# Kernel tuning notes

Hardware: AMD Instinct MI355X
Metric: run time of the kernel (lower is better)

## Reference

```python
import jax, jax.numpy as jnp
import numpy as np

VOCAB, EMBED, HID = 10, 256, 512
B, S, T = 8, 1024, 256  # Senc = S // 4 = 256


def _conv1d(x, w, b):
    # x: (B, Cin, L), w: (Cout, Cin, 3), padding=1 -> same length
    y = jax.lax.conv_general_dilated(x, w, window_strides=(1,), padding=[(1, 1)],
                                     dimension_numbers=('NCH', 'OIH', 'NCH'))
    return y + b[None, :, None]


def _maxpool2(x):
    # MaxPool1d(kernel=2, stride=2) on (B, C, L)
    b, c, l = x.shape
    return x.reshape(b, c, l // 2, 2).max(axis=-1)


def _lstm_layer(x, wih, whh, bih, bhh):
    # x: (B, T, Din); PyTorch gate order i, f, g, o; zero initial state
    b, t, _ = x.shape
    h_dim = whh.shape[1]
    xg = x @ wih.T + (bih + bhh)  # (B, T, 4H) - input projection hoisted out of scan

    def step(carry, xt):
        h, c = carry
        gates = xt + h @ whh.T
        i, f, g, o = jnp.split(gates, 4, axis=-1)
        c = jax.nn.sigmoid(f) * c + jax.nn.sigmoid(i) * jnp.tanh(g)
        h = jax.nn.sigmoid(o) * jnp.tanh(c)
        return (h, c), h

    init = (jnp.zeros((b, h_dim), x.dtype), jnp.zeros((b, h_dim), x.dtype))
    _, hs = jax.lax.scan(step, init, jnp.swapaxes(xg, 0, 1))
    return jnp.swapaxes(hs, 0, 1)  # (B, T, H)


def setup_inputs() -> dict:
    key = jax.random.key(0)
    ks = jax.random.split(key, 24)

    def unif(k, shape, fan_in):
        bound = 1.0 / np.sqrt(fan_in)
        return jax.random.uniform(k, shape, jnp.float32, -bound, bound)

    inp = {
        'src': jax.random.randint(ks[0], (B, S), 0, VOCAB),
        'tgt': jax.random.randint(ks[1], (B, T), 0, VOCAB),
        'embedding': jax.random.normal(ks[2], (VOCAB, EMBED), jnp.float32),
        'conv1_w': unif(ks[3], (256, EMBED, 3), EMBED * 3),
        'conv1_b': unif(ks[4], (256,), EMBED * 3),
        'conv2_w': unif(ks[5], (512, 256, 3), 256 * 3),
        'conv2_b': unif(ks[6], (512,), 256 * 3),
        'conv3_w': unif(ks[7], (512, 512, 3), 512 * 3),
        'conv3_b': unif(ks[8], (512,), 512 * 3),
        'lstm0_wih': unif(ks[9], (4 * HID, EMBED), HID),
        'lstm0_whh': unif(ks[10], (4 * HID, HID), HID),
        'lstm0_bih': unif(ks[11], (4 * HID,), HID),
        'lstm0_bhh': unif(ks[12], (4 * HID,), HID),
        'lstm1_wih': unif(ks[13], (4 * HID, HID), HID),
        'lstm1_whh': unif(ks[14], (4 * HID, HID), HID),
        'lstm1_bih': unif(ks[15], (4 * HID,), HID),
        'lstm1_bhh': unif(ks[16], (4 * HID,), HID),
        'attn_w': unif(ks[17], (1, 2 * HID), 2 * HID),
        'attn_b': unif(ks[18], (1,), 2 * HID),
        'out_w': unif(ks[19], (VOCAB, HID), HID),
        'out_b': unif(ks[20], (VOCAB,), HID),
    }
    return inp


def reference(src, tgt, embedding, conv1_w, conv1_b, conv2_w, conv2_b, conv3_w, conv3_b,
              lstm0_wih, lstm0_whh, lstm0_bih, lstm0_bhh,
              lstm1_wih, lstm1_whh, lstm1_bih, lstm1_bhh,
              attn_w, attn_b, out_w, out_b):
    # --- CNN encoder ---
    x = jnp.swapaxes(embedding[src], 1, 2)          # (B, E, S)
    x = _maxpool2(jax.nn.relu(_conv1d(x, conv1_w, conv1_b)))
    x = _maxpool2(jax.nn.relu(_conv1d(x, conv2_w, conv2_b)))
    x = jax.nn.relu(_conv1d(x, conv3_w, conv3_b))
    enc = jnp.swapaxes(x, 1, 2)                     # (B, Senc, 512)

    # --- LSTM decoder (2 layers) ---
    h = _lstm_layer(embedding[tgt], lstm0_wih, lstm0_whh, lstm0_bih, lstm0_bhh)
    dec = _lstm_layer(h, lstm1_wih, lstm1_whh, lstm1_bih, lstm1_bhh)  # (B, T, 512)

    # --- Bahdanau-style attention ---
    # Linear(cat([dec, enc])) == dec @ W[:, :H].T + enc @ W[:, H:].T + b,
    # so broadcast the two rank-1 projections instead of materializing (B,T,Senc,1024).
    dec_p = jnp.einsum('bth,h->bt', dec, attn_w[0, :HID])   # (B, T)
    enc_p = jnp.einsum('bsh,h->bs', enc, attn_w[0, HID:])   # (B, Senc)
    scores = dec_p[:, :, None] + enc_p[:, None, :] + attn_b[0]  # (B, T, Senc)
    attn = jax.nn.softmax(scores, axis=2)
    context = jnp.einsum('bts,bsd->btd', attn, enc)         # (B, T, 512)

    output = dec @ out_w.T + out_b                          # (B, T, VOCAB)
    # Original module computes context then discards it; we return it too so the
    # attention workload is not dead-code-eliminated under jit.
    return output, context
```

## Files before the change

### kernel.cpp

```cpp
#include <hip/hip_runtime.h>
#include <cstddef>

constexpr int OXB0 = 0;
constexpr int OXB1 = OXB0 + 8 * 1026 * 256;
constexpr int OXB2 = OXB1 + 8 * 514 * 256;
constexpr int OENC = OXB2 + 8 * 258 * 512;
constexpr int OWR1 = OENC + 8 * 256 * 512;
constexpr int OWR2 = OWR1 + 768 * 256;
constexpr int OWR3 = OWR2 + 768 * 512;
constexpr int OWR0 = OWR3 + 1536 * 512;
constexpr int OTGT = OWR0 + 256 * 2048;
constexpr int OXG0 = OTGT + 2048 * 256;
constexpr int OH0S = OXG0 + 2048 * 2048;
constexpr int OH1S = OH0S + 257 * 4096;
constexpr int OCTX = OH1S + 257 * 4096;
constexpr int OFLG = OCTX + 8 * 512;

constexpr int FSTR = 16;
constexpr unsigned SENT = 0x7FC0DEADu;

__device__ __forceinline__ float hsum4(const float4& a) { return a.x + a.y + a.z + a.w; }
__device__ __forceinline__ float4 relu4(float4 v, const float4& bv) {
    v.x = fmaxf(v.x + bv.x, 0.f); v.y = fmaxf(v.y + bv.y, 0.f);
    v.z = fmaxf(v.z + bv.z, 0.f); v.w = fmaxf(v.w + bv.w, 0.f); return v;
}
__device__ __forceinline__ float4 max4(const float4& a, const float4& b) {
    float4 r; r.x = fmaxf(a.x, b.x); r.y = fmaxf(a.y, b.y);
    r.z = fmaxf(a.z, b.z); r.w = fmaxf(a.w, b.w); return r;
}
__device__ __forceinline__ float sigmf(float x) { return 1.f / (1.f + expf(-x)); }
__device__ __forceinline__ void fma4(float4& acc, const float4& a, const float4& b) {
    acc.x = fmaf(a.x, b.x, acc.x); acc.y = fmaf(a.y, b.y, acc.y);
    acc.z = fmaf(a.z, b.z, acc.z); acc.w = fmaf(a.w, b.w, acc.w);
}

__device__ __forceinline__ unsigned long long aload64(const float* p) {
    return __hip_atomic_load((const unsigned long long*)p, __ATOMIC_RELAXED,
                             __HIP_MEMORY_SCOPE_AGENT);
}
__device__ __forceinline__ void astore32(float* p, float v) {
    __hip_atomic_store((unsigned int*)p, __float_as_uint(v), __ATOMIC_RELAXED,
                       __HIP_MEMORY_SCOPE_AGENT);
}
__device__ __forceinline__ int aloadi(const int* p) {
    return __hip_atomic_load(p, __ATOMIC_RELAXED, __HIP_MEMORY_SCOPE_AGENT);
}
__device__ __forceinline__ void astorei(int* p, int v) {
    __hip_atomic_store(p, v, __ATOMIC_RELAXED, __HIP_MEMORY_SCOPE_AGENT);
}
__device__ __forceinline__ float2 unpack64(unsigned long long v) {
    float2 f;
    f.x = __uint_as_float((unsigned)v);
    f.y = __uint_as_float((unsigned)(v >> 32));
    return f;
}
__device__ __forceinline__ unsigned sent_in(unsigned long long v) {
    return ((unsigned)v == SENT) | ((unsigned)(v >> 32) == SENT);
}

__global__ void init_kernel(float* __restrict__ ws, int* __restrict__ flags) {
    int idx = blockIdx.x * 256 + threadIdx.x;
    int stride = gridDim.x * 256;
    float sentf = __uint_as_float(SENT);
    for (int i = idx; i < 257 * 4096; i += stride) {
        float v = (i < 4096) ? 0.f : sentf;
        ws[OH0S + i] = v;
        ws[OH1S + i] = v;
    }
    for (int i = idx; i < 192 * FSTR; i += stride) flags[i] = 0;
    for (int i = idx; i < 8 * 2 * 256; i += stride) {
        int b = i >> 9, rr = (i >> 8) & 1, c = i & 255;
        ws[OXB1 + b * 131584 + (rr ? 513 : 0) * 256 + c] = 0.f;
    }
    for (int i = idx; i < 8 * 2 * 512; i += stride) {
        int b = i >> 10, rr = (i >> 9) & 1, c = i & 511;
        ws[OXB2 + b * 132096 + (rr ? 257 : 0) * 512 + c] = 0.f;
    }
}

__global__ void embed_src_kernel(const int* __restrict__ src, const float* __restrict__ emb,
                                 float* __restrict__ xb0) {
    int fi = blockIdx.x * 256 + threadIdx.x;
    int e4 = fi & 63;
    int r = fi >> 6;
    int b = r / 1026;
    int p = r - b * 1026;
    float4 v = make_float4(0.f, 0.f, 0.f, 0.f);
    if (p > 0 && p < 1025) {
        int row = src[b * 1024 + (p - 1)];
        v = *(const float4*)(emb + row * 256 + e4 * 4);
    }
    *(float4*)(xb0 + (size_t)fi * 4) = v;
}

__global__ void gather_tgt_kernel(const int* __restrict__ tgt, const float* __restrict__ emb,
                                  float* __restrict__ et) {
    int fi = blockIdx.x * 256 + threadIdx.x;
    int e4 = fi & 63;
    int r = fi >> 6;
    int t = r >> 3, b = r & 7;
    int row = tgt[b * 256 + t];
    *(float4*)(et + (size_t)fi * 4) = *(const float4*)(emb + row * 256 + e4 * 4);
}

__global__ void tr_conv_kernel(const float* __restrict__ w, float* __restrict__ wr,
                               int Cout, int Cin) {
    int idx = blockIdx.x * 256 + threadIdx.x;
    int co = idx / (Cin * 3);
    int rem = idx - co * Cin * 3;
    int ci = rem / 3;
    int dk = rem - ci * 3;
    wr[(dk * Cin + ci) * Cout + co] = w[idx];
}
__global__ void tr_mat_kernel(const float* __restrict__ w, float* __restrict__ wr,
                              int N, int K) {
    int idx = blockIdx.x * 256 + threadIdx.x;
    int n = idx / K;
    int k = idx - n * K;
    wr[k * N + n] = w[idx];
}

__launch_bounds__(256)
__global__ void gemm_kernel(const float* __restrict__ A, int aBS, int RS, int K,
                            const float* __restrict__ Bw, int N,
                            const float* __restrict__ bias, const float* __restrict__ bias2,
                            float* __restrict__ out, int oBS, int mode) {
    __shared__ float As[32 * 68];
    __shared__ float Bs[32 * 64];
    const int tid = threadIdx.x;
    const int tl = tid & 15, tco = tid >> 4;
    const int m0 = blockIdx.x * 64, n0 = blockIdx.y * 64;
    const int b = blockIdx.z;
    const float* Ab = A + (size_t)b * aBS;
    float4 acc0 = make_float4(0, 0, 0, 0), acc1 = acc0, acc2 = acc0, acc3 = acc0;

    for (int k0 = 0; k0 < K; k0 += 32) {
#pragma unroll
        for (int p = 0; p < 2; ++p) {
            int f = p * 256 + tid;
            int row = f >> 3, j4 = f & 7;
            float4 av = *(const float4*)(Ab + (size_t)(m0 + row) * RS + k0 + j4 * 4);
            int kb = j4 * 4;
            As[(kb + 0) * 68 + row] = av.x;
            As[(kb + 1) * 68 + row] = av.y;
            As[(kb + 2) * 68 + row] = av.z;
            As[(kb + 3) * 68 + row] = av.w;
        }
#pragma unroll
        for (int p = 0; p < 2; ++p) {
            int f = p * 256 + tid;
            int kk = f >> 4, j4 = f & 15;
            *(float4*)(&Bs[kk * 64 + j4 * 4]) =
                *(const float4*)(Bw + (size_t)(k0 + kk) * N + n0 + j4 * 4);
        }
        __syncthreads();
#pragma unroll
        for (int kk = 0; kk < 32; ++kk) {
            float4 a4 = *(const float4*)(&As[kk * 68 + tl * 4]);
            float4 b4 = *(const float4*)(&Bs[kk * 64 + tco * 4]);
            acc0.x = fmaf(a4.x, b4.x, acc0.x); acc0.y = fmaf(a4.x, b4.y, acc0.y);
            acc0.z = fmaf(a4.x, b4.z, acc0.z); acc0.w = fmaf(a4.x, b4.w, acc0.w);
            acc1.x = fmaf(a4.y, b4.x, acc1.x); acc1.y = fmaf(a4.y, b4.y, acc1.y);
            acc1.z = fmaf(a4.y, b4.z, acc1.z); acc1.w = fmaf(a4.y, b4.w, acc1.w);
            acc2.x = fmaf(a4.z, b4.x, acc2.x); acc2.y = fmaf(a4.z, b4.y, acc2.y);
            acc2.z = fmaf(a4.z, b4.z, acc2.z); acc2.w = fmaf(a4.z, b4.w, acc2.w);
            acc3.x = fmaf(a4.w, b4.x, acc3.x); acc3.y = fmaf(a4.w, b4.y, acc3.y);
            acc3.z = fmaf(a4.w, b4.z, acc3.z); acc3.w = fmaf(a4.w, b4.w, acc3.w);
        }
        __syncthreads();
    }

    int nb = n0 + tco * 4;
    float4 bv;
    bv.x = bias[nb + 0]; bv.y = bias[nb + 1]; bv.z = bias[nb + 2]; bv.w = bias[nb + 3];
    if (bias2) { bv.x += bias2[nb + 0]; bv.y += bias2[nb + 1]; bv.z += bias2[nb + 2]; bv.w += bias2[nb + 3]; }

    if (mode == 0) {
        float4 v0 = acc0, v1 = acc1, v2 = acc2, v3 = acc3;
        v0.x += bv.x; v0.y += bv.y; v0.z += bv.z; v0.w += bv.w;
        v1.x += bv.x; v1.y += bv.y; v1.z += bv.z; v1.w += bv.w;
        v2.x += bv.x; v2.y += bv.y; v2.z += bv.z; v2.w += bv.w;
        v3.x += bv.x; v3.y += bv.y; v3.z += bv.z; v3.w += bv.w;
        int mr = m0 + tl * 4;
        *(float4*)(out + (size_t)(mr + 0) * N + nb) = v0;
        *(float4*)(out + (size_t)(mr + 1) * N + nb) = v1;
        *(float4*)(out + (size_t)(mr + 2) * N + nb) = v2;
        *(float4*)(out + (size_t)(mr + 3) * N + nb) = v3;
    } else if (mode == 1) {
        float4 v0 = relu4(acc0, bv), v1 = relu4(acc1, bv), v2 = relu4(acc2, bv), v3 = relu4(acc3, bv);
        float4 p0 = max4(v0, v1), p1 = max4(v2, v3);
        int lout = (m0 + tl * 4) >> 1;
        float* ob = out + (size_t)b * oBS + (size_t)(1 + lout) * N + nb;
        *(float4*)ob = p0;
        *(float4*)(ob + N) = p1;
    } else {
        float4 v0 = relu4(acc0, bv), v1 = relu4(acc1, bv), v2 = relu4(acc2, bv), v3 = relu4(acc3, bv);
        int mr = m0 + tl * 4;
        float* ob = out + (size_t)b * oBS + (size_t)mr * N + nb;
        *(float4*)(ob + 0 * N) = v0;
        *(float4*)(ob + 1 * N) = v1;
        *(float4*)(ob + 2 * N) = v2;
        *(float4*)(ob + 3 * N) = v3;
    }
}

__launch_bounds__(256, 1)
__global__ void lstm_kernel(const float* __restrict__ xg0,
                            const float* __restrict__ whh0,
                            const float* __restrict__ wih1,
                            const float* __restrict__ whh1,
                            const float* __restrict__ bih1,
                            const float* __restrict__ bhh1,
                            float* __restrict__ h0s, float* __restrict__ h1s,
                            int* __restrict__ flags) {
    const int tid = threadIdx.x;
    const int wg = blockIdx.x;

    if (wg < 64) {
        const int wg0 = wg;
        const int cg = tid >> 6;
        const int bg = (tid >> 5) & 1;
        const int ks = tid & 31;
        float2 W2[4][2][8];
#pragma unroll
        for (int g = 0; g < 4; ++g)
#pragma unroll
            for (int e = 0; e < 2; ++e) {
                const float* wr = whh0 + (size_t)(g * 512 + wg0 * 8 + cg * 2 + e) * 512 + ks * 2;
#pragma unroll
                for (int q = 0; q < 8; ++q)
                    W2[g][e][q] = *(const float2*)(wr + q * 64);
            }
        const int vg = ks >> 3, ve = (ks >> 2) & 1, vbi = ks & 3;
        const int vb = bg * 4 + vbi;
        const size_t xgoff = (size_t)vb * 2048 + vg * 512 + wg0 * 8 + cg * 2 + ve;
        const int ob = bg * 4 + (ks & 3);
        const int ou = cg * 2 + ((ks >> 2) & 1);
        float cst = 0.f;

        for (int t = 0; t < 256; ++t) {
            float xgv = xg0[(size_t)t * 16384 + xgoff];
            if (t > 0 && tid < 64) {
                int gd = 1 << 20;
                while (aloadi(&flags[tid * FSTR]) < t && --gd) {}
            }
            __syncthreads();
            unsigned long long hv[4][8];
            int gd = 1 << 16;
            for (;;) {
#pragma unroll
                for (int bi = 0; bi < 4; ++bi) {
                    const float* hb = h0s + (size_t)t * 4096 + (bg * 4 + bi) * 512 + ks * 2;
#pragma unroll
                    for (int q = 0; q < 8; ++q)
                        hv[bi][q] = aload64(hb + q * 64);
                }
                unsigned bad = 0;
#pragma unroll
                for (int bi = 0; bi < 4; ++bi)
#pragma unroll
                    for (int q = 0; q < 8; ++q) bad |= sent_in(hv[bi][q]);
                if (!__any((int)bad) || --gd <= 0) break;
            }
            float2 acc[4][2][4];
#pragma unroll
            for (int g = 0; g < 4; ++g)
#pragma unroll
                for (int e = 0; e < 2; ++e)
#pragma unroll
                    for (int bi = 0; bi < 4; ++bi) acc[g][e][bi] = make_float2(0.f, 0.f);
#pragma unroll
            for (int q = 0; q < 8; ++q)
#pragma unroll
                for (int bi = 0; bi < 4; ++bi) {
                    float2 h2 = unpack64(hv[bi][q]);
#pragma unroll
                    for (int g = 0; g < 4; ++g)
#pragma unroll
                        for (int e = 0; e < 2; ++e) {
                            acc[g][e][bi].x = fmaf(W2[g][e][q].x, h2.x, acc[g][e][bi].x);
                            acc[g][e][bi].y = fmaf(W2[g][e][q].y, h2.y, acc[g][e][bi].y);
                        }
                }
            float s[32];
#pragma unroll
            for (int g = 0; g < 4; ++g)
#pragma unroll
                for (int e = 0; e < 2; ++e)
#pragma unroll
                    for (int bi = 0; bi < 4; ++bi)
                        s[g * 8 + e * 4 + bi] = acc[g][e][bi].x + acc[g][e][bi].y;
#pragma unroll
            for (int i = 0; i < 16; ++i) {
                float t_ = (ks & 16) ? s[i] : s[i + 16];
                float k_ = (ks & 16) ? s[i + 16] : s[i];
                s[i] = k_ + __shfl_xor(t_, 16);
            }
#pragma unroll
            for (int i = 0; i < 8; ++i) {
                float t_ = (ks & 8) ? s[i] : s[i + 8];
                float k_ = (ks & 8) ? s[i + 8] : s[i];
                s[i] = k_ + __shfl_xor(t_, 8);
            }
#pragma unroll
            for (int i = 0; i < 4; ++i) {
                float t_ = (ks & 4) ? s[i] : s[i + 4];
                float k_ = (ks & 4) ? s[i + 4] : s[i];
                s[i] = k_ + __shfl_xor(t_, 4);
            }
#pragma unroll
            for (int i = 0; i < 2; ++i) {
                float t_ = (ks & 2) ? s[i] : s[i + 2];
                float k_ = (ks & 2) ? s[i + 2] : s[i];
                s[i] = k_ + __shfl_xor(t_, 2);
            }
            {
                float t_ = (ks & 1) ? s[0] : s[1];
                float k_ = (ks & 1) ? s[1] : s[0];
                s[0] = k_ + __shfl_xor(t_, 1);
            }
            float red = s[0] + xgv;
            float fgv = __shfl_xor(red, 8);
            float ggv = __shfl_xor(red, 16);
            float ogv = __shfl_xor(red, 24);
            if (ks < 8) {
                cst = sigmf(fgv) * cst + sigmf(red) * tanhf(ggv);
                float hval = sigmf(ogv) * tanhf(cst);
                astore32(h0s + (size_t)(t + 1) * 4096 + ob * 512 + wg0 * 8 + ou, hval);
            }
            __syncthreads();
            if (tid == 0) astorei(&flags[wg0 * FSTR], t + 1);
        }
    } else {
        const int wg1 = wg - 64;
        const int w = tid >> 6;
        const int cg = w >> 1, bgv = w & 1;
        const int ks = tid & 63;
        float2 W2[4][2][8];
#pragma unroll
        for (int g = 0; g < 4; ++g)
#pragma unroll
            for (int e = 0; e < 2; ++e) {
                const size_t ro = (size_t)(g * 512 + wg1 * 4 + cg * 2 + e) * 512 + ks * 2;
#pragma unroll
                for (int q = 0; q < 4; ++q)
                    W2[g][e][q] = *(const float2*)(wih1 + ro + q * 128);
#pragma unroll
                for (int q = 4; q < 8; ++q)
                    W2[g][e][q] = *(const float2*)(whh1 + ro + (q - 4) * 128);
            }
        const int vg = (((ks >> 5) & 1) << 1) | ((ks >> 3) & 1);
        const int ve = (ks >> 2) & 1, vbi = ks & 3;
        const int rv = vg * 512 + wg1 * 4 + cg * 2 + ve;
        const float biasv = bih1[rv] + bhh1[rv];
        const int ob = bgv * 4 + (ks & 3);
        const int ou = cg * 2 + ((ks >> 2) & 1);
        float cst = 0.f;

        for (int t = 0; t < 256; ++t) {
            if (tid < 64) {
                int gd = 1 << 20;
                while (aloadi(&flags[tid * FSTR]) < t + 1 && --gd) {}
            } else if (tid < 192 && t > 0) {
                int gd = 1 << 20;
                while (aloadi(&flags[tid * FSTR]) < t && --gd) {}
            }
            __syncthreads();
            unsigned long long hv[4][8];
            int gd = 1 << 16;
            for (;;) {
#pragma unroll
                for (int bi = 0; bi < 4; ++bi) {
                    const float* h0b = h0s + (size_t)(t + 1) * 4096 + (bgv * 4 + bi) * 512 + ks * 2;
                    const float* h1b = h1s + (size_t)t * 4096 + (bgv * 4 + bi) * 512 + ks * 2;
#pragma unroll
                    for (int q = 0; q < 4; ++q) hv[bi][q] = aload64(h0b + q * 128);
#pragma unroll
                    for (int q = 4; q < 8; ++q) hv[bi][q] = aload64(h1b + (q - 4) * 128);
                }
                unsigned bad = 0;
#pragma unroll
                for (int bi = 0; bi < 4; ++bi)
#pragma unroll
                    for (int q = 0; q < 8; ++q) bad |= sent_in(hv[bi][q]);
                if (!__any((int)bad) || --gd <= 0) break;
            }
            float2 acc[4][2][4];
#pragma unroll
            for (int g = 0; g < 4; ++g)
#pragma unroll
                for (int e = 0; e < 2; ++e)
#pragma unroll
                    for (int bi = 0; bi < 4; ++bi) acc[g][e][bi] = make_float2(0.f, 0.f);
#pragma unroll
            for (int q = 0; q < 8; ++q)
#pragma unroll
                for (int bi = 0; bi < 4; ++bi) {
                    float2 h2 = unpack64(hv[bi][q]);
#pragma unroll
                    for (int g = 0; g < 4; ++g)
#pragma unroll
                        for (int e = 0; e < 2; ++e) {
                            acc[g][e][bi].x = fmaf(W2[g][e][q].x, h2.x, acc[g][e][bi].x);
                            acc[g][e][bi].y = fmaf(W2[g][e][q].y, h2.y, acc[g][e][bi].y);
                        }
                }
            float s[32];
#pragma unroll
            for (int g = 0; g < 4; ++g)
#pragma unroll
                for (int e = 0; e < 2; ++e)
#pragma unroll
                    for (int bi = 0; bi < 4; ++bi)
                        s[g * 8 + e * 4 + bi] = acc[g][e][bi].x + acc[g][e][bi].y;
#pragma unroll
            for (int i = 0; i < 16; ++i) {
                float t_ = (ks & 32) ? s[i] : s[i + 16];
                float k_ = (ks & 32) ? s[i + 16] : s[i];
                s[i] = k_ + __shfl_xor(t_, 32);
            }
#pragma unroll
            for (int i = 0; i < 8; ++i) {
                float t_ = (ks & 8) ? s[i] : s[i + 8];
                float k_ = (ks & 8) ? s[i + 8] : s[i];
                s[i] = k_ + __shfl_xor(t_, 8);
            }
#pragma unroll
            for (int i = 0; i < 4; ++i) {
                float t_ = (ks & 4) ? s[i] : s[i + 4];
                float k_ = (ks & 4) ? s[i + 4] : s[i];
                s[i] = k_ + __shfl_xor(t_, 4);
            }
#pragma unroll
            for (int i = 0; i < 2; ++i) {
                float t_ = (ks & 2) ? s[i] : s[i + 2];
                float k_ = (ks & 2) ? s[i + 2] : s[i];
                s[i] = k_ + __shfl_xor(t_, 2);
            }
            {
                float t_ = (ks & 1) ? s[0] : s[1];
                float k_ = (ks & 1) ? s[1] : s[0];
                s[0] = k_ + __shfl_xor(t_, 1);
            }
            s[0] += __shfl_xor(s[0], 16);
            float red = s[0] + biasv;
            float fgv = __shfl_xor(red, 8);
            float ggv = __shfl_xor(red, 32);
            float ogv = __shfl_xor(red, 40);
            if (ks < 8) {
                cst = sigmf(fgv) * cst + sigmf(red) * tanhf(ggv);
                float hval = sigmf(ogv) * tanhf(cst);
                astore32(h1s + (size_t)(t + 1) * 4096 + ob * 512 + wg1 * 4 + ou, hval);
            }
            __syncthreads();
            if (tid == 0) astorei(&flags[(64 + wg1) * FSTR], t + 1);
        }
    }
}

__launch_bounds__(256)
__global__ void attn_kernel(const float* __restrict__ enc, const float* __restrict__ attn_w,
                            float* __restrict__ ctx) {
    __shared__ float aw[512];
    __shared__ float pr[256];
    __shared__ float red[8];
    const int b = blockIdx.x, tid = threadIdx.x;
    if (tid < 128) ((float4*)aw)[tid] = ((const float4*)(attn_w + 512))[tid];
    __syncthreads();
    const float* er = enc + (size_t)(b * 256 + tid) * 512;
    float4 a4 = make_float4(0, 0, 0, 0);
#pragma unroll 8
    for (int i = 0; i < 128; ++i) {
        float4 e4 = *(const float4*)(er + i * 4);
        float4 w4 = *(const float4*)(aw + i * 4);
        fma4(a4, e4, w4);
    }
    float v = hsum4(a4);
    float m = v;
#pragma unroll
    for (int off = 32; off > 0; off >>= 1) m = fmaxf(m, __shfl_xor(m, off));
    if ((tid & 63) == 0) red[tid >> 6] = m;
    __syncthreads();
    if (tid == 0) red[4] = fmaxf(fmaxf(red[0], red[1]), fmaxf(red[2], red[3]));
    __syncthreads();
    float e = expf(v - red[4]);
    pr[tid] = e;
    float s = e;
#pragma unroll
    for (int off = 32; off > 0; off >>= 1) s += __shfl_xor(s, off);
    if ((tid & 63) == 0) red[tid >> 6] = s;
    __syncthreads();
    if (tid == 0) red[5] = red[0] + red[1] + red[2] + red[3];
    __syncthreads();
    float inv = 1.f / red[5];
    for (int hh = tid; hh < 512; hh += 256) {
        float acc = 0.f;
#pragma unroll 8
        for (int s2 = 0; s2 < 256; ++s2)
            acc = fmaf(pr[s2], enc[(size_t)(b * 256 + s2) * 512 + hh], acc);
        ctx[b * 512 + hh] = acc * inv;
    }
}

__global__ void bcast_ctx_kernel(const float* __restrict__ ctx, float* __restrict__ outc) {
    int fi = blockIdx.x * 256 + threadIdx.x;
    int h4 = fi & 127;
    int b = fi >> 15;
    ((float4*)outc)[fi] = ((const float4*)ctx)[b * 128 + h4];
}

__launch_bounds__(256)
__global__ void out_proj_kernel(const float* __restrict__ h1s, const float* __restrict__ ow,
                                const float* __restrict__ ob, float* __restrict__ out) {
    int lane = threadIdx.x & 63;
    int m = blockIdx.x * 4 + (threadIdx.x >> 6);
    int t = m >> 3, b = m & 7;
    const float* dr = h1s + (size_t)(t + 1) * 4096 + b * 512 + lane * 8;
    float4 d0 = *(const float4*)dr;
    float4 d1 = *(const float4*)(dr + 4);
    float acc[10];
#pragma unroll
    for (int v = 0; v < 10; ++v) {
        const float* wr = ow + v * 512 + lane * 8;
        float4 w0 = *(const float4*)wr, w1 = *(const float4*)(wr + 4);
        acc[v] = d0.x * w0.x + d0.y * w0.y + d0.z * w0.z + d0.w * w0.w +
                 d1.x * w1.x + d1.y * w1.y + d1.z * w1.z + d1.w * w1.w;
    }
#pragma unroll
    for (int v = 0; v < 10; ++v)
#pragma unroll
        for (int off = 32; off > 0; off >>= 1) acc[v] += __shfl_xor(acc[v], off);
    if (lane == 0) {
        float* o = out + (size_t)(b * 256 + t) * 10;
#pragma unroll
        for (int v = 0; v < 10; ++v) o[v] = acc[v] + ob[v];
    }
}

extern "C" void kernel_launch(void* const* d_in, const int* in_sizes, int n_in,
                              void* d_out, int out_size, void* d_ws, size_t ws_size,
                              hipStream_t stream) {
    const int* src = (const int*)d_in[0];
    const int* tgt = (const int*)d_in[1];
    const float* emb = (const float*)d_in[2];
    const float* c1w = (const float*)d_in[3];
    const float* c1b = (const float*)d_in[4];
    const float* c2w = (const float*)d_in[5];
    const float* c2b = (const float*)d_in[6];
    const float* c3w = (const float*)d_in[7];
    const float* c3b = (const float*)d_in[8];
    const float* wih0 = (const float*)d_in[9];
    const float* whh0 = (const float*)d_in[10];
    const float* bih0 = (const float*)d_in[11];
    const float* bhh0 = (const float*)d_in[12];
    const float* wih1 = (const float*)d_in[13];
    const float* whh1 = (const float*)d_in[14];
    const float* bih1 = (const float*)d_in[15];
    const float* bhh1 = (const float*)d_in[16];
    const float* attn_w = (const float*)d_in[17];
    const float* out_w = (const float*)d_in[19];
    const float* out_b = (const float*)d_in[20];

    float* ws = (float*)d_ws;
    float* xb0 = ws + OXB0;
    float* xb1 = ws + OXB1;
    float* xb2 = ws + OXB2;
    float* enc = ws + OENC;
    float* wr1 = ws + OWR1;
    float* wr2 = ws + OWR2;
    float* wr3 = ws + OWR3;
    float* wr0 = ws + OWR0;
    float* etg = ws + OTGT;
    float* xg0 = ws + OXG0;
    float* h0s = ws + OH0S;
    float* h1s = ws + OH1S;
    float* ctx = ws + OCTX;
    int* flags = (int*)(ws + OFLG);
    float* outp = (float*)d_out;

    init_kernel<<<1024, 256, 0, stream>>>(ws, flags);
    embed_src_kernel<<<2052, 256, 0, stream>>>(src, emb, xb0);
    gather_tgt_kernel<<<512, 256, 0, stream>>>(tgt, emb, etg);
    tr_conv_kernel<<<768, 256, 0, stream>>>(c1w, wr1, 256, 256);
    tr_conv_kernel<<<1536, 256, 0, stream>>>(c2w, wr2, 512, 256);
    tr_conv_kernel<<<3072, 256, 0, stream>>>(c3w, wr3, 512, 512);
    tr_mat_kernel<<<2048, 256, 0, stream>>>(wih0, wr0, 2048, 256);

    gemm_kernel<<<dim3(32, 32, 1), 256, 0, stream>>>(etg, 0, 256, 256, wr0, 2048,
                                                     bih0, bhh0, xg0, 0, 0);
    gemm_kernel<<<dim3(16, 4, 8), 256, 0, stream>>>(xb0, 262656, 256, 768, wr1, 256,
                                                    c1b, nullptr, xb1, 131584, 1);
    gemm_kernel<<<dim3(8, 8, 8), 256, 0, stream>>>(xb1, 131584, 256, 768, wr2, 512,
                                                   c2b, nullptr, xb2, 132096, 1);
    gemm_kernel<<<dim3(4, 8, 8), 256, 0, stream>>>(xb2, 132096, 512, 1536, wr3, 512,
                                                   c3b, nullptr, enc, 131072, 2);
    lstm_kernel<<<192, 256, 0, stream>>>(xg0, whh0, wih1, whh1, bih1, bhh1,
                                         h0s, h1s, flags);
    attn_kernel<<<8, 256, 0, stream>>>(enc, attn_w, ctx);
    bcast_ctx_kernel<<<1024, 256, 0, stream>>>(ctx, outp + 20480);
    out_proj_kernel<<<512, 256, 0, stream>>>(h1s, out_w, out_b, outp);
}
```

Baseline: 1.414 ms.

## Run conv encoder and attention concurrently with LSTM in one fused persistent kernel

Moves the source embedding, conv weight transposes, three conv GEMMs, attention and context broadcast into 64 extra workgroups of the LSTM kernel. These run alongside the latency-bound LSTM recurrence, and the stages are ordered with atomic counters acting as grid barriers. The aim is to hide the encoder work behind the serial LSTM and remove several kernel launches. The risks are contention for CUs and memory bandwidth with the LSTM workgroups, and a spin-wait that relies on all 256 blocks being co-resident.

```diff
diff --git a/kernel.cpp b/kernel.cpp
--- a/kernel.cpp
+++ b/kernel.cpp
@@ -15,6 +15,7 @@
 constexpr int OH1S = OH0S + 257 * 4096;
 constexpr int OCTX = OH1S + 257 * 4096;
 constexpr int OFLG = OCTX + 8 * 512;
+constexpr int OCNT = OFLG + 192 * 16;
 
 constexpr int FSTR = 16;
 constexpr unsigned SENT = 0x7FC0DEADu;
@@ -58,7 +59,23 @@
     return ((unsigned)v == SENT) | ((unsigned)(v >> 32) == SENT);
 }
 
-__global__ void init_kernel(float* __restrict__ ws, int* __restrict__ flags) {
+__device__ __forceinline__ void stage_signal(int* cnt) {
+    asm volatile("s_waitcnt vmcnt(0)" ::: "memory");
+    __syncthreads();
+    if (threadIdx.x == 0)
+        __hip_atomic_fetch_add(cnt, 1, __ATOMIC_RELEASE, __HIP_MEMORY_SCOPE_AGENT);
+}
+__device__ __forceinline__ void stage_wait(int* cnt, int target) {
+    if (threadIdx.x == 0) {
+        int gd = 1 << 22;
+        while (__hip_atomic_load(cnt, __ATOMIC_RELAXED, __HIP_MEMORY_SCOPE_AGENT) < target && --gd) {}
+        (void)__hip_atomic_load(cnt, __ATOMIC_ACQUIRE, __HIP_MEMORY_SCOPE_AGENT);
+    }
+    __syncthreads();
+}
+
+__global__ void init_kernel(float* __restrict__ ws, int* __restrict__ flags,
+                            int* __restrict__ cnts) {
     int idx = blockIdx.x * 256 + threadIdx.x;
     int stride = gridDim.x * 256;
     float sentf = __uint_as_float(SENT);
@@ -68,6 +85,7 @@
         ws[OH1S + i] = v;
     }
     for (int i = idx; i < 192 * FSTR; i += stride) flags[i] = 0;
+    for (int i = idx; i < 8; i += stride) cnts[i] = 0;
     for (int i = idx; i < 8 * 2 * 256; i += stride) {
         int b = i >> 9, rr = (i >> 8) & 1, c = i & 255;
         ws[OXB1 + b * 131584 + (rr ? 513 : 0) * 256 + c] = 0.f;
@@ -76,21 +94,6 @@
         int b = i >> 10, rr = (i >> 9) & 1, c = i & 511;
         ws[OXB2 + b * 132096 + (rr ? 257 : 0) * 512 + c] = 0.f;
     }
-}
-
-__global__ void embed_src_kernel(const int* __restrict__ src, const float* __restrict__ emb,
-                                 float* __restrict__ xb0) {
-    int fi = blockIdx.x * 256 + threadIdx.x;
-    int e4 = fi & 63;
-    int r = fi >> 6;
-    int b = r / 1026;
-    int p = r - b * 1026;
-    float4 v = make_float4(0.f, 0.f, 0.f, 0.f);
-    if (p > 0 && p < 1025) {
-        int row = src[b * 1024 + (p - 1)];
-        v = *(const float4*)(emb + row * 256 + e4 * 4);
-    }
-    *(float4*)(xb0 + (size_t)fi * 4) = v;
 }
 
 __global__ void gather_tgt_kernel(const int* __restrict__ tgt, const float* __restrict__ emb,
@@ -103,15 +106,6 @@
     *(float4*)(et + (size_t)fi * 4) = *(const float4*)(emb + row * 256 + e4 * 4);
 }
 
-__global__ void tr_conv_kernel(const float* __restrict__ w, float* __restrict__ wr,
-                               int Cout, int Cin) {
-    int idx = blockIdx.x * 256 + threadIdx.x;
-    int co = idx / (Cin * 3);
-    int rem = idx - co * Cin * 3;
-    int ci = rem / 3;
-    int dk = rem - ci * 3;
-    wr[(dk * Cin + ci) * Cout + co] = w[idx];
-}
 __global__ void tr_mat_kernel(const float* __restrict__ w, float* __restrict__ wr,
                               int N, int K) {
     int idx = blockIdx.x * 256 + threadIdx.x;
@@ -120,18 +114,15 @@
     wr[k * N + n] = w[idx];
 }
 
-__launch_bounds__(256)
-__global__ void gemm_kernel(const float* __restrict__ A, int aBS, int RS, int K,
-                            const float* __restrict__ Bw, int N,
-                            const float* __restrict__ bias, const float* __restrict__ bias2,
-                            float* __restrict__ out, int oBS, int mode) {
-    __shared__ float As[32 * 68];
-    __shared__ float Bs[32 * 64];
+__device__ void gemm_tile(const float* __restrict__ A, int aBS, int RS, int K,
+                          const float* __restrict__ Bw, int N,
+                          const float* __restrict__ bias, const float* __restrict__ bias2,
+                          float* __restrict__ out, int oBS, int mode,
+                          int bx, int by, int bz, float* As, float* Bs) {
     const int tid = threadIdx.x;
     const int tl = tid & 15, tco = tid >> 4;
-    const int m0 = blockIdx.x * 64, n0 = blockIdx.y * 64;
-    const int b = blockIdx.z;
-    const float* Ab = A + (size_t)b * aBS;
+    const int m0 = bx * 64, n0 = by * 64;
+    const float* Ab = A + (size_t)bz * aBS;
     float4 acc0 = make_float4(0, 0, 0, 0), acc1 = acc0, acc2 = acc0, acc3 = acc0;
 
     for (int k0 = 0; k0 < K; k0 += 32) {
@@ -190,13 +181,13 @@
         float4 v0 = relu4(acc0, bv), v1 = relu4(acc1, bv), v2 = relu4(acc2, bv), v3 = relu4(acc3, bv);
         float4 p0 = max4(v0, v1), p1 = max4(v2, v3);
         int lout = (m0 + tl * 4) >> 1;
-        float* ob = out + (size_t)b * oBS + (size_t)(1 + lout) * N + nb;
+        float* ob = out + (size_t)bz * oBS + (size_t)(1 + lout) * N + nb;
         *(float4*)ob = p0;
         *(float4*)(ob + N) = p1;
     } else {
         float4 v0 = relu4(acc0, bv), v1 = relu4(acc1, bv), v2 = relu4(acc2, bv), v3 = relu4(acc3, bv);
         int mr = m0 + tl * 4;
-        float* ob = out + (size_t)b * oBS + (size_t)mr * N + nb;
+        float* ob = out + (size_t)bz * oBS + (size_t)mr * N + nb;
         *(float4*)(ob + 0 * N) = v0;
         *(float4*)(ob + 1 * N) = v1;
         *(float4*)(ob + 2 * N) = v2;
@@ -204,15 +195,35 @@
     }
 }
 
+__launch_bounds__(256)
+__global__ void gemm_kernel(const float* __restrict__ A, int aBS, int RS, int K,
+                            const float* __restrict__ Bw, int N,
+                            const float* __restrict__ bias, const float* __restrict__ bias2,
+                            float* __restrict__ out, int oBS, int mode) {
+    __shared__ float As[32 * 68];
+    __shared__ float Bs[32 * 64];
+    gemm_tile(A, aBS, RS, K, Bw, N, bias, bias2, out, oBS, mode,
+              blockIdx.x, blockIdx.y, blockIdx.z, As, Bs);
+}
+
 __launch_bounds__(256, 1)
-__global__ void lstm_kernel(const float* __restrict__ xg0,
-                            const float* __restrict__ whh0,
-                            const float* __restrict__ wih1,
-                            const float* __restrict__ whh1,
-                            const float* __restrict__ bih1,
-                            const float* __restrict__ bhh1,
-                            float* __restrict__ h0s, float* __restrict__ h1s,
-                            int* __restrict__ flags) {
+__global__ void lstm_fused_kernel(const float* __restrict__ xg0,
+                                  const float* __restrict__ whh0,
+                                  const float* __restrict__ wih1,
+                                  const float* __restrict__ whh1,
+                                  const float* __restrict__ bih1,
+                                  const float* __restrict__ bhh1,
+                                  float* __restrict__ h0s, float* __restrict__ h1s,
+                                  int* __restrict__ flags, int* __restrict__ cnts,
+                                  const int* __restrict__ src,
+                                  const float* __restrict__ emb,
+                                  const float* __restrict__ c1w, const float* __restrict__ c1b,
+                                  const float* __restrict__ c2w, const float* __restrict__ c2b,
+                                  const float* __restrict__ c3w, const float* __restrict__ c3b,
+                                  const float* __restrict__ attn_w,
+                                  float* __restrict__ ws, float* __restrict__ outp) {
+    __shared__ float As[32 * 68];
+    __shared__ float Bs[32 * 64];
     const int tid = threadIdx.x;
     const int wg = blockIdx.x;
 
@@ -331,7 +342,7 @@
             __syncthreads();
             if (tid == 0) astorei(&flags[wg0 * FSTR], t + 1);
         }
-    } else {
+    } else if (wg < 192) {
         const int wg1 = wg - 64;
         const int w = tid >> 6;
         const int cg = w >> 1, bgv = w & 1;
@@ -455,58 +466,118 @@
             __syncthreads();
             if (tid == 0) astorei(&flags[(64 + wg1) * FSTR], t + 1);
         }
-    }
-}
-
-__launch_bounds__(256)
-__global__ void attn_kernel(const float* __restrict__ enc, const float* __restrict__ attn_w,
-                            float* __restrict__ ctx) {
-    __shared__ float aw[512];
-    __shared__ float pr[256];
-    __shared__ float red[8];
-    const int b = blockIdx.x, tid = threadIdx.x;
-    if (tid < 128) ((float4*)aw)[tid] = ((const float4*)(attn_w + 512))[tid];
-    __syncthreads();
-    const float* er = enc + (size_t)(b * 256 + tid) * 512;
-    float4 a4 = make_float4(0, 0, 0, 0);
+    } else {
+        const int eb = wg - 192;
+        const int gidx = eb * 256 + tid;
+        float* xb0 = ws + OXB0;
+        float* xb1 = ws + OXB1;
+        float* xb2 = ws + OXB2;
+        float* enc = ws + OENC;
+        float* wr1 = ws + OWR1;
+        float* wr2 = ws + OWR2;
+        float* wr3 = ws + OWR3;
+        float* ctx = ws + OCTX;
+
+        for (int fi = gidx; fi < 8 * 1026 * 64; fi += 16384) {
+            int e4 = fi & 63;
+            int r = fi >> 6;
+            int b = r / 1026;
+            int p = r - b * 1026;
+            float4 v = make_float4(0.f, 0.f, 0.f, 0.f);
+            if (p > 0 && p < 1025) {
+                int row = src[b * 1024 + (p - 1)];
+                v = *(const float4*)(emb + row * 256 + e4 * 4);
+            }
+            *(float4*)(xb0 + (size_t)fi * 4) = v;
+        }
+        for (int i = gidx; i < 256 * 256 * 3; i += 16384) {
+            int co = i / (256 * 3); int rem = i - co * 256 * 3;
+            int ci = rem / 3; int dk = rem - ci * 3;
+            wr1[(dk * 256 + ci) * 256 + co] = c1w[i];
+        }
+        for (int i = gidx; i < 512 * 256 * 3; i += 16384) {
+            int co = i / (256 * 3); int rem = i - co * 256 * 3;
+            int ci = rem / 3; int dk = rem - ci * 3;
+            wr2[(dk * 256 + ci) * 512 + co] = c2w[i];
+        }
+        for (int i = gidx; i < 512 * 512 * 3; i += 16384) {
+            int co = i / (512 * 3); int rem = i - co * 512 * 3;
+            int ci = rem / 3; int dk = rem - ci * 3;
+            wr3[(dk * 512 + ci) * 512 + co] = c3w[i];
+        }
+        stage_signal(&cnts[0]);
+        stage_wait(&cnts[0], 64);
+        for (int j = 0; j < 8; ++j) {
+            int t = eb * 8 + j;
+            gemm_tile(xb0, 262656, 256, 768, wr1, 256, c1b, nullptr, xb1, 131584, 1,
+                      t & 15, (t >> 4) & 3, t >> 6, As, Bs);
+        }
+        stage_signal(&cnts[1]);
+        stage_wait(&cnts[1], 64);
+        for (int j = 0; j < 8; ++j) {
+            int t = eb * 8 + j;
+            gemm_tile(xb1, 131584, 256, 768, wr2, 512, c2b, nullptr, xb2, 132096, 1,
+                      t & 7, (t >> 3) & 7, t >> 6, As, Bs);
+        }
+        stage_signal(&cnts[2]);
+        stage_wait(&cnts[2], 64);
+        for (int j = 0; j < 4; ++j) {
+            int t = eb * 4 + j;
+            gemm_tile(xb2, 132096, 512, 1536, wr3, 512, c3b, nullptr, enc, 131072, 2,
+                      t & 3, (t >> 2) & 7, t >> 5, As, Bs);
+        }
+        stage_signal(&cnts[3]);
+        stage_wait(&cnts[3], 64);
+        if (eb < 8) {
+            float* aw = As;
+            float* pr = As + 512;
+            float* red = As + 768;
+            const int b = eb;
+            if (tid < 128) ((float4*)aw)[tid] = ((const float4*)(attn_w + 512))[tid];
+            __syncthreads();
+            const float* er = enc + (size_t)(b * 256 + tid) * 512;
+            float4 a4 = make_float4(0, 0, 0, 0);
 #pragma unroll 8
-    for (int i = 0; i < 128; ++i) {
-        float4 e4 = *(const float4*)(er + i * 4);
-        float4 w4 = *(const float4*)(aw + i * 4);
-        fma4(a4, e4, w4);
-    }
-    float v = hsum4(a4);
-    float m = v;
-#pragma unroll
-    for (int off = 32; off > 0; off >>= 1) m = fmaxf(m, __shfl_xor(m, off));
-    if ((tid & 63) == 0) red[tid >> 6] = m;
-    __syncthreads();
-    if (tid == 0) red[4] = fmaxf(fmaxf(red[0], red[1]), fmaxf(red[2], red[3]));
-    __syncthreads();
-    float e = expf(v - red[4]);
-    pr[tid] = e;
-    float s = e;
-#pragma unroll
-    for (int off = 32; off > 0; off >>= 1) s += __shfl_xor(s, off);
-    if ((tid & 63) == 0) red[tid >> 6] = s;
-    __syncthreads();
-    if (tid == 0) red[5] = red[0] + red[1] + red[2] + red[3];
-    __syncthreads();
-    float inv = 1.f / red[5];
-    for (int hh = tid; hh < 512; hh += 256) {
-        float acc = 0.f;
+            for (int i = 0; i < 128; ++i) {
+                float4 e4 = *(const float4*)(er + i * 4);
+                float4 w4 = *(const float4*)(aw + i * 4);
+                fma4(a4, e4, w4);
+            }
+            float v = hsum4(a4);
+            float m = v;
+#pragma unroll
+            for (int off = 32; off > 0; off >>= 1) m = fmaxf(m, __shfl_xor(m, off));
+            if ((tid & 63) == 0) red[tid >> 6] = m;
+            __syncthreads();
+            if (tid == 0) red[4] = fmaxf(fmaxf(red[0], red[1]), fmaxf(red[2], red[3]));
+            __syncthreads();
+            float e = expf(v - red[4]);
+            pr[tid] = e;
+            float sum = e;
+#pragma unroll
+            for (int off = 32; off > 0; off >>= 1) sum += __shfl_xor(sum, off);
+            if ((tid & 63) == 0) red[tid >> 6] = sum;
+            __syncthreads();
+            if (tid == 0) red[5] = red[0] + red[1] + red[2] + red[3];
+            __syncthreads();
+            float inv = 1.f / red[5];
+            for (int hh = tid; hh < 512; hh += 256) {
+                float acc2 = 0.f;
 #pragma unroll 8
-        for (int s2 = 0; s2 < 256; ++s2)
-            acc = fmaf(pr[s2], enc[(size_t)(b * 256 + s2) * 512 + hh], acc);
-        ctx[b * 512 + hh] = acc * inv;
-    }
-}
-
-__global__ void bcast_ctx_kernel(const float* __restrict__ ctx, float* __restrict__ outc) {
-    int fi = blockIdx.x * 256 + threadIdx.x;
-    int h4 = fi & 127;
-    int b = fi >> 15;
-    ((float4*)outc)[fi] = ((const float4*)ctx)[b * 128 + h4];
+                for (int s2 = 0; s2 < 256; ++s2)
+                    acc2 = fmaf(pr[s2], enc[(size_t)(b * 256 + s2) * 512 + hh], acc2);
+                ctx[b * 512 + hh] = acc2 * inv;
+            }
+            stage_signal(&cnts[4]);
+        }
+        stage_wait(&cnts[4], 8);
+        float* outc = outp + 20480;
+        for (int fi = gidx; fi < 262144; fi += 16384) {
+            int h4 = fi & 127;
+            int b = fi >> 15;
+            ((float4*)outc)[fi] = ((const float4*)(ctx))[b * 128 + h4];
+        }
+    }
 }
 
 __launch_bounds__(256)
@@ -562,41 +633,23 @@
     const float* out_b = (const float*)d_in[20];
 
     float* ws = (float*)d_ws;
-    float* xb0 = ws + OXB0;
-    float* xb1 = ws + OXB1;
-    float* xb2 = ws + OXB2;
-    float* enc = ws + OENC;
-    float* wr1 = ws + OWR1;
-    float* wr2 = ws + OWR2;
-    float* wr3 = ws + OWR3;
     float* wr0 = ws + OWR0;
     float* etg = ws + OTGT;
     float* xg0 = ws + OXG0;
     float* h0s = ws + OH0S;
     float* h1s = ws + OH1S;
-    float* ctx = ws + OCTX;
     int* flags = (int*)(ws + OFLG);
+    int* cnts = (int*)(ws + OCNT);
     float* outp = (float*)d_out;
 
-    init_kernel<<<1024, 256, 0, stream>>>(ws, flags);
-    embed_src_kernel<<<2052, 256, 0, stream>>>(src, emb, xb0);
+    init_kernel<<<1024, 256, 0, stream>>>(ws, flags, cnts);
     gather_tgt_kernel<<<512, 256, 0, stream>>>(tgt, emb, etg);
-    tr_conv_kernel<<<768, 256, 0, stream>>>(c1w, wr1, 256, 256);
-    tr_conv_kernel<<<1536, 256, 0, stream>>>(c2w, wr2, 512, 256);
-    tr_conv_kernel<<<3072, 256, 0, stream>>>(c3w, wr3, 512, 512);
     tr_mat_kernel<<<2048, 256, 0, stream>>>(wih0, wr0, 2048, 256);
-
     gemm_kernel<<<dim3(32, 32, 1), 256, 0, stream>>>(etg, 0, 256, 256, wr0, 2048,
                                                      bih0, bhh0, xg0, 0, 0);
-    gemm_kernel<<<dim3(16, 4, 8), 256, 0, stream>>>(xb0, 262656, 256, 768, wr1, 256,
-                                                    c1b, nullptr, xb1, 131584, 1);
-    gemm_kernel<<<dim3(8, 8, 8), 256, 0, stream>>>(xb1, 131584, 256, 768, wr2, 512,
-                                                   c2b, nullptr, xb2, 132096, 1);
-    gemm_kernel<<<dim3(4, 8, 8), 256, 0, stream>>>(xb2, 132096, 512, 1536, wr3, 512,
-                                                   c3b, nullptr, enc, 131072, 2);
-    lstm_kernel<<<192, 256, 0, stream>>>(xg0, whh0, wih1, whh1, bih1, bhh1,
-                                         h0s, h1s, flags);
-    attn_kernel<<<8, 256, 0, stream>>>(enc, attn_w, ctx);
-    bcast_ctx_kernel<<<1024, 256, 0, stream>>>(ctx, outp + 20480);
+    lstm_fused_kernel<<<256, 256, 0, stream>>>(xg0, whh0, wih1, whh1, bih1, bhh1,
+                                               h0s, h1s, flags, cnts,
+                                               src, emb, c1w, c1b, c2w, c2b, c3w, c3b,
+                                               attn_w, ws, outp);
     out_proj_kernel<<<512, 256, 0, stream>>>(h1s, out_w, out_b, outp);
 }
```

Result: no change. 1.405 ms, median of 2 (-0.7%).
